# Performance work log

Measured on AMD Instinct MI355X. Metric: run time of the kernel, lower is better.

## Reference

```python
import jax, jax.numpy as jnp
import numpy as np

N_NODES = 16384
N_EDGES = 262144
N_GRAPHS = 64
COLORS = 16
EMB = 256
HEADS = 8
FFN = 1024
LAYERS = 4
LMAX = 320


def _ln(x, g, b, eps=1e-5):
    m = x.mean(-1, keepdims=True)
    v = x.var(-1, keepdims=True)
    return (x - m) * jax.lax.rsqrt(v + eps) * g + b


def setup_inputs() -> dict:
    key = jax.random.key(0)
    ks = iter(jax.random.split(key, 64))
    s = 0.05
    def rn(shape):
        return jax.random.normal(next(ks), shape, jnp.float32) * s
    # 64 graphs: 32 with 192 nodes, 32 with 320 nodes -> total 16384, L_max=320
    lengths = np.concatenate([np.full(32, 192, np.int64), np.full(32, 320, np.int64)])
    batches = jnp.asarray(np.concatenate([[0], np.cumsum(lengths)]).astype(np.int32))
    x = jax.random.normal(next(ks), (N_NODES, COLORS), jnp.float32)
    edge_index = jax.random.randint(next(ks), (2, N_EDGES), 0, N_NODES, jnp.int32)
    inp = dict(
        x=x, edge_index=edge_index, batches=batches, L_max=LMAX,
        sW0=rn((COLORS, EMB)), sWn0=rn((COLORS, EMB)), sb0=jnp.zeros(EMB),
        sW1=rn((EMB, EMB)), sWn1=rn((EMB, EMB)), sb1=jnp.zeros(EMB),
        sW2=rn((EMB, EMB)), sWn2=rn((EMB, EMB)), sb2=jnp.zeros(EMB),
        Wq=rn((LAYERS, EMB, EMB)), Wk=rn((LAYERS, EMB, EMB)), Wv=rn((LAYERS, EMB, EMB)),
        bq=jnp.zeros((LAYERS, EMB)), bk=jnp.zeros((LAYERS, EMB)), bv=jnp.zeros((LAYERS, EMB)),
        Wo=rn((LAYERS, EMB, EMB)), bo=jnp.zeros((LAYERS, EMB)),
        ln1g=jnp.ones((LAYERS, EMB)), ln1b=jnp.zeros((LAYERS, EMB)),
        ln2g=jnp.ones((LAYERS, EMB)), ln2b=jnp.zeros((LAYERS, EMB)),
        W1=rn((LAYERS, EMB, FFN)), b1=jnp.zeros((LAYERS, FFN)),
        W2=rn((LAYERS, FFN, EMB)), b2=jnp.zeros((LAYERS, EMB)),
    )
    return inp


def reference(x, edge_index, batches, L_max,
              sW0, sWn0, sb0, sW1, sWn1, sb1, sW2, sWn2, sb2,
              Wq, Wk, Wv, bq, bk, bv, Wo, bo,
              ln1g, ln1b, ln2g, ln2b, W1, b1, W2, b2):
    N = x.shape[0]
    src, dst = edge_index[0], edge_index[1]
    deg = jnp.maximum(
        jax.ops.segment_sum(jnp.ones(src.shape[0], x.dtype), dst, num_segments=N), 1.0
    )[:, None]

    def sage(h, Ws, Wn, b, act):
        agg = jax.ops.segment_sum(h[src], dst, num_segments=N) / deg  # mean neighbor agg
        h2 = h @ Ws + agg @ Wn + b
        return jax.nn.relu(h2) if act else h2

    z = sage(x, sW0, sWn0, sb0, True)
    z = sage(z, sW1, sWn1, sb1, True)
    z = sage(z, sW2, sWn2, sb2, False)

    # pack_and_pad (intended semantics): seq-first [L_max, n_graphs, D] + key padding mask
    nG = batches.shape[0] - 1
    lengths = batches[1:] - batches[:-1]
    ids = jnp.arange(N)
    seg = jnp.searchsorted(batches, ids, side='right') - 1  # graph id per node
    pos = ids - batches[seg]                                 # position within graph
    D = z.shape[1]
    h = jnp.zeros((L_max, nG, D), z.dtype).at[pos, seg].set(z)
    pad = jnp.arange(L_max)[None, :] >= lengths[:, None]     # [nG, L_max], True = padded

    H = HEADS
    dh = D // H
    scale = 1.0 / np.sqrt(dh).astype(np.float32)
    for l in range(Wq.shape[0]):
        L, Bg = h.shape[0], h.shape[1]
        q = (h @ Wq[l] + bq[l]).reshape(L, Bg, H, dh)
        k = (h @ Wk[l] + bk[l]).reshape(L, Bg, H, dh)
        v = (h @ Wv[l] + bv[l]).reshape(L, Bg, H, dh)
        sc = jnp.einsum('lbhd,mbhd->bhlm', q, k) * scale
        sc = jnp.where(pad[:, None, None, :], -1e9, sc)
        a = jax.nn.softmax(sc, axis=-1)
        o = jnp.einsum('bhlm,mbhd->lbhd', a, v).reshape(L, Bg, D) @ Wo[l] + bo[l]
        h = _ln(h + o, ln1g[l], ln1b[l])
        ff = jax.nn.relu(h @ W1[l] + b1[l]) @ W2[l] + b2[l]
        h = _ln(h + ff, ln2g[l], ln2b[l])
    return h
```

## Files before the change

### kernel.cpp

```cpp
#include <hip/hip_runtime.h>
#include <hip/hip_bf16.h>
#include <math.h>

#define NN  16384
#define NE  262144
#define NG  64
#define CIN 16
#define DD  256
#define NHD 8
#define DHD 32
#define DFF 1024
#define NLY 4
#define LM  320
#define QS  768
#define QKW 512
#define NV  16384
#define NRV 16512

typedef __attribute__((ext_vector_type(8))) short bf16x8;
typedef __attribute__((ext_vector_type(4))) float f32x4;

__device__ __forceinline__ unsigned short f2bf(float f) {
    union { __hip_bfloat16 h; unsigned short u; } cv;
    cv.h = __float2bfloat16(f);
    return cv.u;
}
__device__ __forceinline__ float bf2f(unsigned short u) {
    return __uint_as_float((unsigned int)u << 16);
}
__device__ __forceinline__ void gl_lds16(const unsigned short* g, unsigned short* l) {
    __builtin_amdgcn_global_load_lds(
        (const __attribute__((address_space(1))) unsigned int*)g,
        (__attribute__((address_space(3))) unsigned int*)l, 16, 0, 0);
}
__device__ __forceinline__ int gsearch(const int* __restrict__ batches, int row) {
    int lo = 0, hi = NG;
    while (lo < hi) {
        int mid = (lo + hi + 1) >> 1;
        if (batches[mid] <= row) lo = mid; else hi = mid - 1;
    }
    return lo;
}

__global__ __launch_bounds__(256) void prep_all_kernel(
    const float* __restrict__ Wq, const float* __restrict__ Wk, const float* __restrict__ Wv,
    const float* __restrict__ Wo, const float* __restrict__ W1, const float* __restrict__ W2,
    const float* __restrict__ sW1, const float* __restrict__ sWn1,
    const float* __restrict__ sW2, const float* __restrict__ sWn2,
    const float* __restrict__ bq, const float* __restrict__ bk, const float* __restrict__ bv,
    unsigned short* __restrict__ Wqkvt, unsigned short* __restrict__ Wot,
    unsigned short* __restrict__ W1t, unsigned short* __restrict__ W2t,
    unsigned short* __restrict__ sW1t, unsigned short* __restrict__ sWn1t,
    unsigned short* __restrict__ sW2t, unsigned short* __restrict__ sWn2t,
    float* __restrict__ bqkvp,
    uint4* __restrict__ hbz, uint4* __restrict__ obz, int* __restrict__ counts)
{
    const int t = threadIdx.x;
    int bid = blockIdx.x;
    if (bid < 12) {
        int i = bid * 256 + t;
        if (i < NLY * QS) {
            int n = i % QS, l = i / QS;
            const float* b = (n < 256) ? bq : (n < 512 ? bk : bv);
            float v = b[l * DD + (n & 255)];
            if (n < 256) v *= 0.17677669529663687f;
            bqkvp[i] = v;
        }
        return;
    }
    bid -= 12;
    if (bid >= 832) {
        int i = (bid - 832) * 256 + t;
        if (i < 4096) {
            hbz[i] = (uint4){0u, 0u, 0u, 0u};
            obz[i] = (uint4){0u, 0u, 0u, 0u};
        }
        if (i < NN) counts[i] = 0;
        return;
    }
    __shared__ float Ls[64][68];
    const float* inP;
    unsigned short* outP;
    int strideIn, strideOut;
    float sc = 1.f;
    if (bid < 192) {
        int x = bid % 12, y = (bid / 12) % 4, l = bid / 48;
        int n0 = x * 64, k0 = y * 64;
        const float* W = (n0 < 256) ? Wq : (n0 < 512 ? Wk : Wv);
        if (n0 < 256) sc = 0.17677669529663687f;
        inP  = W + ((size_t)l * DD + k0) * DD + (n0 & 255);
        strideIn = DD;
        outP = Wqkvt + ((size_t)l * QS + n0) * DD + k0;
        strideOut = DD;
    } else if (bid < 192 + 64) {
        bid -= 192;
        int x = bid % 4, y = (bid / 4) % 4, l = bid / 16;
        int n0 = x * 64, k0 = y * 64;
        inP  = Wo + ((size_t)l * DD + k0) * DD + n0;
        strideIn = DD;
        outP = Wot + ((size_t)l * DD + n0) * DD + k0;
        strideOut = DD;
    } else if (bid < 192 + 64 + 256) {
        bid -= 192 + 64;
        int x = bid % 16, y = (bid / 16) % 4, l = bid / 64;
        int n0 = x * 64, k0 = y * 64;
        inP  = W1 + ((size_t)l * DD + k0) * DFF + n0;
        strideIn = DFF;
        outP = W1t + ((size_t)l * DFF + n0) * DD + k0;
        strideOut = DD;
    } else if (bid < 192 + 64 + 512) {
        bid -= 192 + 64 + 256;
        int x = bid % 4, y = (bid / 4) % 16, l = bid / 64;
        int n0 = x * 64, k0 = y * 64;
        inP  = W2 + ((size_t)l * DFF + k0) * DD + n0;
        strideIn = DD;
        outP = W2t + ((size_t)l * DD + n0) * DFF + k0;
        strideOut = DFF;
    } else {
        bid -= 192 + 64 + 512;
        int w = bid / 16, r = bid % 16;
        int x = r % 4, y = r / 4;
        int n0 = x * 64, k0 = y * 64;
        const float* src = (w == 0) ? sW1 : (w == 1) ? sWn1 : (w == 2) ? sW2 : sWn2;
        unsigned short* dst = (w == 0) ? sW1t : (w == 1) ? sWn1t : (w == 2) ? sW2t : sWn2t;
        inP  = src + (size_t)k0 * DD + n0;
        strideIn = DD;
        outP = dst + (size_t)n0 * DD + k0;
        strideOut = DD;
    }
    #pragma unroll
    for (int it = 0; it < 4; ++it) {
        int lin = it * 256 + t;
        int kr = lin >> 4, nc = (lin & 15) * 4;
        float4 v = *(const float4*)&inP[(size_t)kr * strideIn + nc];
        Ls[kr][nc]     = v.x * sc;
        Ls[kr][nc + 1] = v.y * sc;
        Ls[kr][nc + 2] = v.z * sc;
        Ls[kr][nc + 3] = v.w * sc;
    }
    __syncthreads();
    #pragma unroll
    for (int it = 0; it < 2; ++it) {
        int lin = it * 256 + t;
        int nr = lin >> 3, kc = (lin & 7) * 8;
        unsigned short pk[8];
        #pragma unroll
        for (int j = 0; j < 8; ++j) pk[j] = f2bf(Ls[kc + j][nr]);
        *(uint4*)&outP[(size_t)nr * strideOut + kc] = *(uint4*)pk;
    }
}

__global__ void count_edges_kernel(const int* __restrict__ dst, int* __restrict__ counts) {
    int e = blockIdx.x * 256 + threadIdx.x;
    if (e < NE) atomicAdd(&counts[dst[e]], 1);
}

__global__ __launch_bounds__(1024) void scan_kernel(const int* __restrict__ counts,
                                                    int* __restrict__ offsets,
                                                    int* __restrict__ cursor) {
    __shared__ int part[1024];
    int t = threadIdx.x;
    int base = t * 16;
    int s = 0;
    #pragma unroll
    for (int i = 0; i < 16; ++i) s += counts[base + i];
    part[t] = s;
    __syncthreads();
    for (int off = 1; off < 1024; off <<= 1) {
        int val = (t >= off) ? part[t - off] : 0;
        __syncthreads();
        part[t] += val;
        __syncthreads();
    }
    int run = (t == 0) ? 0 : part[t - 1];
    #pragma unroll
    for (int i = 0; i < 16; ++i) {
        offsets[base + i] = run;
        cursor[base + i]  = run;
        run += counts[base + i];
    }
    if (t == 1023) offsets[NN] = run;
}

__global__ void fill_csr_kernel(const int* __restrict__ src, const int* __restrict__ dst,
                                int* __restrict__ cursor, int* __restrict__ csr) {
    int e = blockIdx.x * 256 + threadIdx.x;
    if (e < NE) {
        int p = atomicAdd(&cursor[dst[e]], 1);
        csr[p] = src[e];
    }
}

__global__ __launch_bounds__(256) void agg_mean16_kernel(
    const float* __restrict__ h, const int* __restrict__ offsets,
    const int* __restrict__ csr, float* __restrict__ out)
{
    int node = blockIdx.x * 16 + (threadIdx.x >> 4);
    int d = threadIdx.x & 15;
    int beg = offsets[node], end = offsets[node + 1];
    float acc = 0.f;
    int e = beg;
    for (; e + 3 < end; e += 4) {
        float v0 = h[(size_t)csr[e] * CIN + d];
        float v1 = h[(size_t)csr[e + 1] * CIN + d];
        float v2 = h[(size_t)csr[e + 2] * CIN + d];
        float v3 = h[(size_t)csr[e + 3] * CIN + d];
        acc += (v0 + v1) + (v2 + v3);
    }
    for (; e < end; ++e) acc += h[(size_t)csr[e] * CIN + d];
    int dg = end - beg; if (dg < 1) dg = 1;
    out[(size_t)node * CIN + d] = acc * (1.f / (float)dg);
}

__global__ __launch_bounds__(256) void agg_mean_b_kernel(
    const unsigned short* __restrict__ h, const int* __restrict__ offsets,
    const int* __restrict__ csr, unsigned short* __restrict__ out)
{
    int node = blockIdx.x * 4 + (threadIdx.x >> 6);
    int lane = threadIdx.x & 63;
    int half = lane >> 5;
    int hl   = lane & 31;
    int beg = offsets[node], end = offsets[node + 1];
    float a[8] = {0.f, 0.f, 0.f, 0.f, 0.f, 0.f, 0.f, 0.f};
    int e = beg + half;
    for (; e + 6 < end; e += 8) {
        bf16x8 h0 = *(const bf16x8*)(h + (size_t)csr[e]     * DD + hl * 8);
        bf16x8 h1 = *(const bf16x8*)(h + (size_t)csr[e + 2] * DD + hl * 8);
        bf16x8 h2 = *(const bf16x8*)(h + (size_t)csr[e + 4] * DD + hl * 8);
        bf16x8 h3 = *(const bf16x8*)(h + (size_t)csr[e + 6] * DD + hl * 8);
        #pragma unroll
        for (int j = 0; j < 8; ++j)
            a[j] += (bf2f((unsigned short)h0[j]) + bf2f((unsigned short)h1[j]))
                  + (bf2f((unsigned short)h2[j]) + bf2f((unsigned short)h3[j]));
    }
    for (; e < end; e += 2) {
        bf16x8 h0 = *(const bf16x8*)(h + (size_t)csr[e] * DD + hl * 8);
        #pragma unroll
        for (int j = 0; j < 8; ++j) a[j] += bf2f((unsigned short)h0[j]);
    }
    #pragma unroll
    for (int j = 0; j < 8; ++j) a[j] += __shfl_xor(a[j], 32, 64);
    int dg = end - beg; if (dg < 1) dg = 1;
    float inv = 1.f / (float)dg;
    if (half == 0) {
        unsigned short pk[8];
        #pragma unroll
        for (int j = 0; j < 8; ++j) pk[j] = f2bf(a[j] * inv);
        *(uint4*)(out + (size_t)node * DD + hl * 8) = *(uint4*)pk;
    }
}

template <int ACT, bool DUAL>
__global__ __launch_bounds__(256) void gemm_f32b_kernel(
    const float* __restrict__ A, const float* __restrict__ W,
    const float* __restrict__ A2, const float* __restrict__ W2,
    const float* __restrict__ bias, unsigned short* __restrict__ Cb,
    int M, int N, int K)
{
    __shared__ __align__(16) float As[16][64];
    __shared__ __align__(16) float Ws[16][64];
    const int t  = threadIdx.x;
    const int tx = t & 15, ty = t >> 4;
    const int m0 = blockIdx.y * 64, n0 = blockIdx.x * 64;
    const int arow = t >> 2, acol = (t & 3) * 4;
    const int wrow = t >> 4, wcol = (t & 15) * 4;
    float acc[4][4] = {};
    const int npass = DUAL ? 2 : 1;
    for (int pass = 0; pass < npass; ++pass) {
        const float* Ap = (DUAL && pass) ? A2 : A;
        const float* Wp = (DUAL && pass) ? W2 : W;
        for (int k0 = 0; k0 < K; k0 += 16) {
            __syncthreads();
            float4 av = *(const float4*)(Ap + (size_t)(m0 + arow) * K + k0 + acol);
            As[acol + 0][arow] = av.x;
            As[acol + 1][arow] = av.y;
            As[acol + 2][arow] = av.z;
            As[acol + 3][arow] = av.w;
            *(float4*)&Ws[wrow][wcol] = *(const float4*)(Wp + (size_t)(k0 + wrow) * N + n0 + wcol);
            __syncthreads();
            #pragma unroll
            for (int kk = 0; kk < 16; ++kk) {
                float4 a4 = *(const float4*)&As[kk][ty * 4];
                float4 b4 = *(const float4*)&Ws[kk][tx * 4];
                float aa[4] = {a4.x, a4.y, a4.z, a4.w};
                float bb[4] = {b4.x, b4.y, b4.z, b4.w};
                #pragma unroll
                for (int i = 0; i < 4; ++i)
                    #pragma unroll
                    for (int j = 0; j < 4; ++j)
                        acc[i][j] += aa[i] * bb[j];
            }
        }
    }
    float4 bv = *(const float4*)(bias + n0 + tx * 4);
    float bb4[4] = {bv.x, bv.y, bv.z, bv.w};
    #pragma unroll
    for (int i = 0; i < 4; ++i) {
        float c[4];
        #pragma unroll
        for (int j = 0; j < 4; ++j) {
            c[j] = acc[i][j] + bb4[j];
            if (ACT == 1) c[j] = fmaxf(c[j], 0.f);
        }
        ushort4 ov;
        ov.x = f2bf(c[0]); ov.y = f2bf(c[1]); ov.z = f2bf(c[2]); ov.w = f2bf(c[3]);
        *(ushort4*)(Cb + (size_t)(m0 + ty * 4 + i) * N + n0 + tx * 4) = ov;
    }
}

template <int ACT, bool DUAL>
__global__ __launch_bounds__(256) void mfma_gemm_kernel(
    const unsigned short* __restrict__ A,  const unsigned short* __restrict__ Wt,
    const unsigned short* __restrict__ A2, const unsigned short* __restrict__ Wt2,
    const float* __restrict__ bias, unsigned short* __restrict__ Cb,
    int M, int N, int K)
{
    __shared__ __align__(16) unsigned short As[128 * 64];
    __shared__ __align__(16) unsigned short Bs[128 * 64];
    const int t = threadIdx.x;
    const int wave = t >> 6, lane = t & 63;
    const int quad = lane >> 4, r16 = lane & 15;
    const int wr = (wave >> 1) * 64, wc = (wave & 1) * 64;
    const int m0 = blockIdx.y * 128, n0 = blockIdx.x * 128;
    const int srow = t >> 3;
    const int scol = ((t & 7) * 8) ^ ((srow & 7) << 3);
    const int swz  = (r16 & 7) << 3;

    f32x4 acc[4][4];
    #pragma unroll
    for (int i = 0; i < 4; ++i)
        #pragma unroll
        for (int j = 0; j < 4; ++j)
            acc[i][j] = (f32x4){0.f, 0.f, 0.f, 0.f};

    const int npass = DUAL ? 2 : 1;
    for (int pass = 0; pass < npass; ++pass) {
        const unsigned short* Ap = (DUAL && pass) ? A2 : A;
        const unsigned short* Wp = (DUAL && pass) ? Wt2 : Wt;
        for (int k0 = 0; k0 < K; k0 += 64) {
            __syncthreads();
            #pragma unroll
            for (int c = 0; c < 4; ++c) {
                gl_lds16(&Ap[(size_t)(m0 + c * 32 + srow) * K + k0 + scol],
                         As + c * 2048 + wave * 512);
                gl_lds16(&Wp[(size_t)(n0 + c * 32 + srow) * K + k0 + scol],
                         Bs + c * 2048 + wave * 512);
            }
            __syncthreads();
            #pragma unroll
            for (int kk = 0; kk < 2; ++kk) {
                const int cofs = (kk * 32 + quad * 8) ^ swz;
                bf16x8 af[4], bfr[4];
                #pragma unroll
                for (int i = 0; i < 4; ++i)
                    af[i] = *(const bf16x8*)&As[(wr + i * 16 + r16) * 64 + cofs];
                #pragma unroll
                for (int j = 0; j < 4; ++j)
                    bfr[j] = *(const bf16x8*)&Bs[(wc + j * 16 + r16) * 64 + cofs];
                #pragma unroll
                for (int i = 0; i < 4; ++i)
                    #pragma unroll
                    for (int j = 0; j < 4; ++j)
                        acc[i][j] = __builtin_amdgcn_mfma_f32_16x16x32_bf16(
                            af[i], bfr[j], acc[i][j], 0, 0, 0);
            }
        }
    }

    float bcol[4];
    #pragma unroll
    for (int j = 0; j < 4; ++j) bcol[j] = bias[n0 + wc + j * 16 + r16];
    #pragma unroll
    for (int i = 0; i < 4; ++i) {
        const int rowb = m0 + wr + i * 16 + quad * 4;
        #pragma unroll
        for (int rr = 0; rr < 4; ++rr) {
            const size_t rb = (size_t)(rowb + rr) * N;
            #pragma unroll
            for (int j = 0; j < 4; ++j) {
                float v = acc[i][j][rr] + bcol[j];
                if (ACT == 1) v = fmaxf(v, 0.f);
                Cb[rb + n0 + wc + j * 16 + r16] = f2bf(v);
            }
        }
    }
}

__global__ __launch_bounds__(256) void gemm_qkv_kernel(
    const unsigned short* __restrict__ A, const unsigned short* __restrict__ Wt,
    const float* __restrict__ bias, const int* __restrict__ batches,
    unsigned short* __restrict__ QKb, unsigned short* __restrict__ Vt, int K)
{
    __shared__ __align__(16) unsigned short As[128 * 64];
    __shared__ __align__(16) unsigned short Bs[128 * 64];
    const int t = threadIdx.x;
    const int wave = t >> 6, lane = t & 63;
    const int quad = lane >> 4, r16 = lane & 15;
    const int wr = (wave >> 1) * 64, wc = (wave & 1) * 64;
    const int m0 = blockIdx.y * 128, n0 = blockIdx.x * 128;
    const int srow = t >> 3;
    const int scol = ((t & 7) * 8) ^ ((srow & 7) << 3);
    const int swz  = (r16 & 7) << 3;

    f32x4 acc[4][4];
    #pragma unroll
    for (int i = 0; i < 4; ++i)
        #pragma unroll
        for (int j = 0; j < 4; ++j)
            acc[i][j] = (f32x4){0.f, 0.f, 0.f, 0.f};

    for (int k0 = 0; k0 < K; k0 += 64) {
        __syncthreads();
        #pragma unroll
        for (int c = 0; c < 4; ++c) {
            gl_lds16(&A[(size_t)(m0 + c * 32 + srow) * K + k0 + scol],
                     As + c * 2048 + wave * 512);
            gl_lds16(&Wt[(size_t)(n0 + c * 32 + srow) * K + k0 + scol],
                     Bs + c * 2048 + wave * 512);
        }
        __syncthreads();
        #pragma unroll
        for (int kk = 0; kk < 2; ++kk) {
            const int cofs = (kk * 32 + quad * 8) ^ swz;
            bf16x8 af[4], bfr[4];
            #pragma unroll
            for (int i = 0; i < 4; ++i)
                af[i] = *(const bf16x8*)&As[(wr + i * 16 + r16) * 64 + cofs];
            #pragma unroll
            for (int j = 0; j < 4; ++j)
                bfr[j] = *(const bf16x8*)&Bs[(wc + j * 16 + r16) * 64 + cofs];
            #pragma unroll
            for (int i = 0; i < 4; ++i)
                #pragma unroll
                for (int j = 0; j < 4; ++j)
                    acc[i][j] = __builtin_amdgcn_mfma_f32_16x16x32_bf16(
                        af[i], bfr[j], acc[i][j], 0, 0, 0);
        }
    }

    float bcol[4];
    #pragma unroll
    for (int j = 0; j < 4; ++j) bcol[j] = bias[n0 + wc + j * 16 + r16];

    if (n0 < 512) {
        #pragma unroll
        for (int i = 0; i < 4; ++i) {
            const int rowb = m0 + wr + i * 16 + quad * 4;
            #pragma unroll
            for (int rr = 0; rr < 4; ++rr) {
                const size_t rb = (size_t)(rowb + rr) * QKW;
                #pragma unroll
                for (int j = 0; j < 4; ++j)
                    QKb[rb + n0 + wc + j * 16 + r16] = f2bf(acc[i][j][rr] + bcol[j]);
            }
        }
    } else {
        #pragma unroll
        for (int i = 0; i < 4; ++i) {
            const int rowb = m0 + wr + i * 16 + quad * 4;
            if (rowb >= NV) continue;
            const int g = gsearch(batches, rowb);
            const int key = rowb - batches[g];
            #pragma unroll
            for (int j = 0; j < 4; ++j) {
                const int dim = n0 - 512 + wc + j * 16 + r16;
                unsigned short pk[4];
                #pragma unroll
                for (int rr = 0; rr < 4; ++rr) pk[rr] = f2bf(acc[i][j][rr] + bcol[j]);
                *(uint2*)&Vt[((size_t)g * DD + dim) * LM + key] = *(uint2*)pk;
            }
        }
    }
}

template <bool PERM>
__global__ __launch_bounds__(512) void gemm_ln_kernel(
    const unsigned short* __restrict__ A, const unsigned short* __restrict__ Wt,
    const float* __restrict__ bias, const unsigned short* __restrict__ residb,
    const float* __restrict__ gam, const float* __restrict__ bet,
    const int* __restrict__ batches,
    float* __restrict__ outF, float* __restrict__ repO,
    unsigned short* __restrict__ outHb, int K)
{
    __shared__ __align__(16) unsigned short As[64 * 64];
    __shared__ __align__(16) unsigned short Bs[256 * 64];
    __shared__ float red[2][4][64];
    const int t = threadIdx.x;
    const int wave = t >> 6, lane = t & 63;
    const int quad = lane >> 4, r16 = lane & 15;
    const int wr = (wave >> 2) * 32;
    const int wc = (wave & 3) * 64;
    const int m0 = blockIdx.x * 64;
    const int srow = t >> 3;
    const int scol = ((t & 7) * 8) ^ ((srow & 7) << 3);
    const int swz  = (r16 & 7) << 3;

    f32x4 acc[2][4];
    #pragma unroll
    for (int i = 0; i < 2; ++i)
        #pragma unroll
        for (int j = 0; j < 4; ++j)
            acc[i][j] = (f32x4){0.f, 0.f, 0.f, 0.f};

    for (int k0 = 0; k0 < K; k0 += 64) {
        __syncthreads();
        gl_lds16(&A[(size_t)(m0 + srow) * K + k0 + scol], As + wave * 512);
        #pragma unroll
        for (int c = 0; c < 4; ++c)
            gl_lds16(&Wt[(size_t)(c * 64 + srow) * K + k0 + scol],
                     Bs + c * 4096 + wave * 512);
        __syncthreads();
        #pragma unroll
        for (int kk = 0; kk < 2; ++kk) {
            const int cofs = (kk * 32 + quad * 8) ^ swz;
            bf16x8 af[2], bfr[4];
            #pragma unroll
            for (int i = 0; i < 2; ++i)
                af[i] = *(const bf16x8*)&As[(wr + i * 16 + r16) * 64 + cofs];
            #pragma unroll
            for (int j = 0; j < 4; ++j)
                bfr[j] = *(const bf16x8*)&Bs[(wc + j * 16 + r16) * 64 + cofs];
            #pragma unroll
            for (int i = 0; i < 2; ++i)
                #pragma unroll
                for (int j = 0; j < 4; ++j)
                    acc[i][j] = __builtin_amdgcn_mfma_f32_16x16x32_bf16(
                        af[i], bfr[j], acc[i][j], 0, 0, 0);
        }
    }

    float bcol[4];
    #pragma unroll
    for (int j = 0; j < 4; ++j) bcol[j] = bias[wc + j * 16 + r16];

    #pragma unroll
    for (int i = 0; i < 2; ++i) {
        const int row = wr + i * 16 + quad * 4;
        #pragma unroll
        for (int rr = 0; rr < 4; ++rr) {
            const size_t rb = (size_t)(m0 + row + rr) * DD;
            float s1 = 0.f, s2 = 0.f;
            #pragma unroll
            for (int j = 0; j < 4; ++j) {
                float v = acc[i][j][rr] + bcol[j] + bf2f(residb[rb + wc + j * 16 + r16]);
                acc[i][j][rr] = v;
                s1 += v;
                s2 += v * v;
            }
            #pragma unroll
            for (int off = 1; off < 16; off <<= 1) {
                s1 += __shfl_xor(s1, off, 64);
                s2 += __shfl_xor(s2, off, 64);
            }
            if (r16 == 0) {
                red[0][wave & 3][row + rr] = s1;
                red[1][wave & 3][row + rr] = s2;
            }
        }
    }
    __syncthreads();

    int gg = 0, posb = 0;
    if (PERM && m0 < NV) {
        gg = gsearch(batches, m0);
        posb = m0 - batches[gg];
    }
    #pragma unroll
    for (int i = 0; i < 2; ++i) {
        const int row = wr + i * 16 + quad * 4;
        #pragma unroll
        for (int rr = 0; rr < 4; ++rr) {
            const int lr = row + rr;
            const int gr = m0 + lr;
            float s1 = red[0][0][lr] + red[0][1][lr] + red[0][2][lr] + red[0][3][lr];
            float s2 = red[1][0][lr] + red[1][1][lr] + red[1][2][lr] + red[1][3][lr];
            float mean = s1 * (1.f / 256.f);
            float var  = s2 * (1.f / 256.f) - mean * mean;
            float rs = rsqrtf(var + 1e-5f);
            const size_t hb = (size_t)gr * DD;
            #pragma unroll
            for (int j = 0; j < 4; ++j) {
                const int col = wc + j * 16 + r16;
                float ov = (acc[i][j][rr] - mean) * rs * gam[col] + bet[col];
                if (PERM) {
                    if (m0 < NV) {
                        outF[((size_t)(posb + lr) * NG + gg) * DD + col] = ov;
                    } else {
                        int g2 = m0 - NV + lr;
                        if (g2 < NG) repO[(size_t)g2 * DD + col] = ov;
                    }
                } else {
                    outHb[hb + col] = f2bf(ov);
                }
            }
        }
    }
}

#define NBT ((NV / 64) * 2)
__global__ __launch_bounds__(256) void attn_kernel(
    const unsigned short* __restrict__ qk, const unsigned short* __restrict__ vt,
    const int* __restrict__ batches, unsigned short* __restrict__ o)
{
    __shared__ __align__(16) unsigned short Pa[4][64 * 40];
    const int bx = blockIdx.x;
    const int tid = threadIdx.x;
    const int wave = tid >> 6;
    const int lane = tid & 63;

    if (bx >= NBT) {
        float* pbuf = (float*)&Pa[wave][0];
        const int idx = (bx - NBT) * 4 + wave;
        const int g = idx >> 3, h = idx & 7;
        const int len = batches[g + 1] - batches[g];
        const size_t gq = (size_t)batches[g];

        float q[32];
        const unsigned short* qrow = qk + (size_t)(NV + g) * QKW + h * 32;
        #pragma unroll
        for (int c = 0; c < 4; ++c) {
            bf16x8 qv = *(const bf16x8*)(qrow + c * 8);
            #pragma unroll
            for (int j = 0; j < 8; ++j) q[c * 8 + j] = bf2f((unsigned short)qv[j]);
        }
        float psum = 0.f;
        for (int key = lane; key < len; key += 64) {
            const unsigned short* krow = qk + (gq + key) * QKW + 256 + h * 32;
            float s = 0.f;
            #pragma unroll
            for (int c = 0; c < 4; ++c) {
                bf16x8 kv = *(const bf16x8*)(krow + c * 8);
                #pragma unroll
                for (int j = 0; j < 8; ++j) s += q[c * 8 + j] * bf2f((unsigned short)kv[j]);
            }
            float pv = __expf(s);
            pbuf[key] = pv;
            psum += pv;
        }
        #pragma unroll
        for (int off = 1; off < 64; off <<= 1) psum += __shfl_xor(psum, off, 64);
        __asm__ volatile("s_waitcnt lgkmcnt(0)" ::: "memory");

        const int d = lane & 31, half = lane >> 5;
        float acc = 0.f;
        const unsigned short* vrow = vt + ((size_t)g * DD + h * 32 + d) * LM;
        for (int key = half * 8; key < len; key += 16) {
            bf16x8 v8 = *(const bf16x8*)(vrow + key);
            #pragma unroll
            for (int j = 0; j < 8; ++j) acc += pbuf[key + j] * bf2f((unsigned short)v8[j]);
        }
        acc += __shfl_xor(acc, 32, 64);
        if (half == 0)
            o[(size_t)(NV + g) * DD + h * 32 + d] = f2bf(acc / psum);
        return;
    }

    const int tile = bx >> 1;
    const int row0 = tile * 64;
    const int h = (bx & 1) * 4 + wave;
    const int quad = lane >> 4, r16 = lane & 15;
    const int g = gsearch(batches, row0);
    const int len = batches[g + 1] - batches[g];
    const size_t gq = (size_t)batches[g];
    unsigned short* pa = Pa[wave];

    bf16x8 qf[4];
    #pragma unroll
    for (int i = 0; i < 4; ++i)
        qf[i] = *(const bf16x8*)(qk + (size_t)(row0 + i * 16 + r16) * QKW + h * 32 + quad * 8);
    bf16x8 onesf;
    #pragma unroll
    for (int j = 0; j < 8; ++j) onesf[j] = (short)0x3F80;

    f32x4 oacc[4][2], lacc[4];
    #pragma unroll
    for (int i = 0; i < 4; ++i) {
        lacc[i] = (f32x4){0.f, 0.f, 0.f, 0.f};
        #pragma unroll
        for (int nt = 0; nt < 2; ++nt)
            oacc[i][nt] = (f32x4){0.f, 0.f, 0.f, 0.f};
    }

    const unsigned short* kbase = qk + gq * QKW + 256 + h * 32 + quad * 8;
    const unsigned short* vbase = vt + ((size_t)g * DD + h * 32 + r16) * LM + quad * 8;

    bf16x8 kf[2], vf[2];
    kf[0] = *(const bf16x8*)(kbase + (size_t)(r16) * QKW);
    kf[1] = *(const bf16x8*)(kbase + (size_t)(16 + r16) * QKW);
    vf[0] = *(const bf16x8*)(vbase);
    vf[1] = *(const bf16x8*)(vbase + 16 * LM);

    for (int t0 = 0; t0 < len; t0 += 32) {
        f32x4 st[2][4];
        #pragma unroll
        for (int mt = 0; mt < 2; ++mt)
            #pragma unroll
            for (int i = 0; i < 4; ++i)
                st[mt][i] = (f32x4){0.f, 0.f, 0.f, 0.f};
        __builtin_amdgcn_s_setprio(1);
        #pragma unroll
        for (int mt = 0; mt < 2; ++mt)
            #pragma unroll
            for (int i = 0; i < 4; ++i)
                st[mt][i] = __builtin_amdgcn_mfma_f32_16x16x32_bf16(
                    kf[mt], qf[i], st[mt][i], 0, 0, 0);
        __builtin_amdgcn_s_setprio(0);

        const bool more = (t0 + 32) < len;
        bf16x8 kn[2], vn[2];
        if (more) {
            const int tn = t0 + 32;
            kn[0] = *(const bf16x8*)(kbase + (size_t)(tn + r16) * QKW);
            kn[1] = *(const bf16x8*)(kbase + (size_t)(tn + 16 + r16) * QKW);
            vn[0] = *(const bf16x8*)(vbase + tn);
            vn[1] = *(const bf16x8*)(vbase + 16 * LM + tn);
        }

        #pragma unroll
        for (int i = 0; i < 4; ++i) {
            #pragma unroll
            for (int mt = 0; mt < 2; ++mt) {
                float pr[4];
                #pragma unroll
                for (int rr = 0; rr < 4; ++rr)
                    pr[rr] = __expf(st[mt][i][rr]);
                uint2 w;
                w.x = ((unsigned)f2bf(pr[1]) << 16) | f2bf(pr[0]);
                w.y = ((unsigned)f2bf(pr[3]) << 16) | f2bf(pr[2]);
                *(uint2*)&pa[(i * 16 + r16) * 40 + mt * 16 + quad * 4] = w;
            }
        }
        __asm__ volatile("s_waitcnt lgkmcnt(0)" ::: "memory");
        bf16x8 pf[4];
        #pragma unroll
        for (int i = 0; i < 4; ++i)
            pf[i] = *(const bf16x8*)&pa[(i * 16 + r16) * 40 + quad * 8];
        __builtin_amdgcn_s_setprio(1);
        #pragma unroll
        for (int i = 0; i < 4; ++i) {
            #pragma unroll
            for (int nt = 0; nt < 2; ++nt)
                oacc[i][nt] = __builtin_amdgcn_mfma_f32_16x16x32_bf16(
                    pf[i], vf[nt], oacc[i][nt], 0, 0, 0);
            lacc[i] = __builtin_amdgcn_mfma_f32_16x16x32_bf16(
                pf[i], onesf, lacc[i], 0, 0, 0);
        }
        __builtin_amdgcn_s_setprio(0);
        if (more) {
            kf[0] = kn[0]; kf[1] = kn[1];
            vf[0] = vn[0]; vf[1] = vn[1];
        }
    }
    #pragma unroll
    for (int i = 0; i < 4; ++i) {
        #pragma unroll
        for (int rr = 0; rr < 4; ++rr) {
            float inv = 1.f / lacc[i][rr];
            size_t base = (size_t)(row0 + i * 16 + quad * 4 + rr) * DD + h * 32;
            #pragma unroll
            for (int nt = 0; nt < 2; ++nt)
                o[base + nt * 16 + r16] = f2bf(oacc[i][nt][rr] * inv);
        }
    }
}

__global__ __launch_bounds__(256) void bcast_pad_kernel(
    const float* __restrict__ repO, const int* __restrict__ batches,
    float* __restrict__ outF)
{
    const int g = blockIdx.x;
    const int t = threadIdx.x;
    const int len = batches[g + 1] - batches[g];
    float v = repO[(size_t)g * DD + t];
    for (int pos = len; pos < LM; ++pos)
        outF[((size_t)pos * NG + g) * DD + t] = v;
}

extern "C" void kernel_launch(void* const* d_in, const int* in_sizes, int n_in,
                              void* d_out, int out_size, void* d_ws, size_t ws_size,
                              hipStream_t stream) {
    const float* x       = (const float*)d_in[0];
    const int*   ei      = (const int*)d_in[1];
    const int*   batches = (const int*)d_in[2];
    const float* sW0  = (const float*)d_in[4];
    const float* sWn0 = (const float*)d_in[5];
    const float* sb0  = (const float*)d_in[6];
    const float* sW1  = (const float*)d_in[7];
    const float* sWn1 = (const float*)d_in[8];
    const float* sb1  = (const float*)d_in[9];
    const float* sW2  = (const float*)d_in[10];
    const float* sWn2 = (const float*)d_in[11];
    const float* sb2  = (const float*)d_in[12];
    const float* Wq   = (const float*)d_in[13];
    const float* Wk   = (const float*)d_in[14];
    const float* Wv   = (const float*)d_in[15];
    const float* bq   = (const float*)d_in[16];
    const float* bk   = (const float*)d_in[17];
    const float* bv   = (const float*)d_in[18];
    const float* Wo   = (const float*)d_in[19];
    const float* bo   = (const float*)d_in[20];
    const float* ln1g = (const float*)d_in[21];
    const float* ln1b = (const float*)d_in[22];
    const float* ln2g = (const float*)d_in[23];
    const float* ln2b = (const float*)d_in[24];
    const float* W1   = (const float*)d_in[25];
    const float* b1   = (const float*)d_in[26];
    const float* W2   = (const float*)d_in[27];
    const float* b2   = (const float*)d_in[28];

    char* p = (char*)d_ws;
    auto alloc = [&](size_t bytes) {
        char* r = p;
        p += (bytes + 255) & ~(size_t)255;
        return r;
    };
    int*   counts  = (int*)alloc((size_t)NN * 4);
    int*   offsets = (int*)alloc((size_t)(NN + 1) * 4);
    int*   cursor  = (int*)alloc((size_t)NN * 4);
    int*   csr     = (int*)alloc((size_t)NE * 4);
    float* agg0    = (float*)alloc((size_t)NN * CIN * 4);
    unsigned short* z0b = (unsigned short*)alloc((size_t)NN * DD * 2);
    unsigned short* a1b = (unsigned short*)alloc((size_t)NN * DD * 2);
    unsigned short* z1b = (unsigned short*)alloc((size_t)NN * DD * 2);
    unsigned short* a2b = (unsigned short*)alloc((size_t)NN * DD * 2);
    unsigned short* Vt = (unsigned short*)alloc((size_t)NG * DD * LM * 2);
    unsigned short* Hb = (unsigned short*)alloc((size_t)NRV * DD * 2);
    unsigned short* Ob = (unsigned short*)alloc((size_t)NRV * DD * 2);
    unsigned short* R  = (unsigned short*)alloc((size_t)NRV * DFF * 2);
    unsigned short* QKb = R;
    unsigned short* F1b = R;
    unsigned short* Wqkvt = (unsigned short*)alloc((size_t)NLY * QS * DD * 2);
    unsigned short* Wot   = (unsigned short*)alloc((size_t)NLY * DD * DD * 2);
    unsigned short* W1t   = (unsigned short*)alloc((size_t)NLY * DFF * DD * 2);
    unsigned short* W2t   = (unsigned short*)alloc((size_t)NLY * DD * DFF * 2);
    unsigned short* sW1t  = (unsigned short*)alloc((size_t)DD * DD * 2);
    unsigned short* sWn1t = (unsigned short*)alloc((size_t)DD * DD * 2);
    unsigned short* sW2t  = (unsigned short*)alloc((size_t)DD * DD * 2);
    unsigned short* sWn2t = (unsigned short*)alloc((size_t)DD * DD * 2);
    float* bqkvp   = (float*)alloc((size_t)NLY * QS * 4);
    float* repOut  = (float*)alloc((size_t)NG * DD * 4);

    prep_all_kernel<<<908, 256, 0, stream>>>(
        Wq, Wk, Wv, Wo, W1, W2, sW1, sWn1, sW2, sWn2, bq, bk, bv,
        Wqkvt, Wot, W1t, W2t, sW1t, sWn1t, sW2t, sWn2t, bqkvp,
        (uint4*)(Hb + (size_t)NV * DD), (uint4*)(Ob + (size_t)NV * DD), counts);

    count_edges_kernel<<<NE / 256, 256, 0, stream>>>(ei + NE, counts);
    scan_kernel<<<1, 1024, 0, stream>>>(counts, offsets, cursor);
    fill_csr_kernel<<<NE / 256, 256, 0, stream>>>(ei, ei + NE, cursor, csr);

    agg_mean16_kernel<<<NN / 16, 256, 0, stream>>>(x, offsets, csr, agg0);
    gemm_f32b_kernel<1, true><<<dim3(DD / 64, NN / 64), 256, 0, stream>>>(
        x, sW0, agg0, sWn0, sb0, z0b, NN, DD, CIN);
    agg_mean_b_kernel<<<NN / 4, 256, 0, stream>>>(z0b, offsets, csr, a1b);
    mfma_gemm_kernel<1, true><<<dim3(DD / 128, NN / 128), 256, 0, stream>>>(
        z0b, sW1t, a1b, sWn1t, sb1, z1b, NN, DD, DD);
    agg_mean_b_kernel<<<NN / 4, 256, 0, stream>>>(z1b, offsets, csr, a2b);
    mfma_gemm_kernel<0, true><<<dim3(DD / 128, NN / 128), 256, 0, stream>>>(
        z1b, sW2t, a2b, sWn2t, sb2, Hb, NN, DD, DD);

    for (int l = 0; l < NLY; ++l) {
        gemm_qkv_kernel<<<dim3(QS / 128, NRV / 128), 256, 0, stream>>>(
            Hb, Wqkvt + (size_t)l * QS * DD, bqkvp + (size_t)l * QS, batches, QKb, Vt, DD);
        attn_kernel<<<NBT + NG * 2, 256, 0, stream>>>(QKb, Vt, batches, Ob);
        gemm_ln_kernel<false><<<NRV / 64, 512, 0, stream>>>(
            Ob, Wot + (size_t)l * DD * DD, bo + (size_t)l * DD, Hb,
            ln1g + (size_t)l * DD, ln1b + (size_t)l * DD, batches, nullptr, nullptr, Hb, DD);
        mfma_gemm_kernel<1, false><<<dim3(DFF / 128, NRV / 128), 256, 0, stream>>>(
            Hb, W1t + (size_t)l * DFF * DD, nullptr, nullptr,
            b1 + (size_t)l * DFF, F1b, NRV, DFF, DD);
        if (l == NLY - 1)
            gemm_ln_kernel<true><<<NRV / 64, 512, 0, stream>>>(
                F1b, W2t + (size_t)l * DD * DFF, b2 + (size_t)l * DD, Hb,
                ln2g + (size_t)l * DD, ln2b + (size_t)l * DD, batches,
                (float*)d_out, repOut, Hb, DFF);
        else
            gemm_ln_kernel<false><<<NRV / 64, 512, 0, stream>>>(
                F1b, W2t + (size_t)l * DD * DFF, b2 + (size_t)l * DD, Hb,
                ln2g + (size_t)l * DD, ln2b + (size_t)l * DD, batches,
                nullptr, nullptr, Hb, DFF);
    }
    bcast_pad_kernel<<<NG, 256, 0, stream>>>(repOut, batches, (float*)d_out);
}
```

Before: 669.5 us.

## Double-buffer LDS tiles in MFMA GEMM kernels to overlap loads with compute

Converts the three MFMA GEMM kernels (generic, QKV, and GEMM+LayerNorm) from single-buffered LDS tiles to ping-pong double buffering. The next K-tile is loaded into LDS with direct global-to-LDS loads while MFMAs run on the current tile. One vmcnt wait plus a barrier per iteration replaces the two __syncthreads. This hides global load latency but doubles LDS use per block (64KB for the 128x128 kernels, larger for the LN kernel), which may reduce occupancy.

```diff
diff --git a/kernel.cpp b/kernel.cpp
--- a/kernel.cpp
+++ b/kernel.cpp
@@ -315,8 +315,8 @@
     const float* __restrict__ bias, unsigned short* __restrict__ Cb,
     int M, int N, int K)
 {
-    __shared__ __align__(16) unsigned short As[128 * 64];
-    __shared__ __align__(16) unsigned short Bs[128 * 64];
+    __shared__ __align__(16) unsigned short As[2][128 * 64];
+    __shared__ __align__(16) unsigned short Bs[2][128 * 64];
     const int t = threadIdx.x;
     const int wave = t >> 6, lane = t & 63;
     const int quad = lane >> 4, r16 = lane & 15;
@@ -325,6 +325,8 @@
     const int srow = t >> 3;
     const int scol = ((t & 7) * 8) ^ ((srow & 7) << 3);
     const int swz  = (r16 & 7) << 3;
+    const int ks = K >> 6;
+    const int nt = DUAL ? ks * 2 : ks;
 
     f32x4 acc[4][4];
     #pragma unroll
@@ -333,38 +335,47 @@
         for (int j = 0; j < 4; ++j)
             acc[i][j] = (f32x4){0.f, 0.f, 0.f, 0.f};
 
-    const int npass = DUAL ? 2 : 1;
-    for (int pass = 0; pass < npass; ++pass) {
-        const unsigned short* Ap = (DUAL && pass) ? A2 : A;
-        const unsigned short* Wp = (DUAL && pass) ? Wt2 : Wt;
-        for (int k0 = 0; k0 < K; k0 += 64) {
-            __syncthreads();
-            #pragma unroll
-            for (int c = 0; c < 4; ++c) {
-                gl_lds16(&Ap[(size_t)(m0 + c * 32 + srow) * K + k0 + scol],
-                         As + c * 2048 + wave * 512);
-                gl_lds16(&Wp[(size_t)(n0 + c * 32 + srow) * K + k0 + scol],
-                         Bs + c * 2048 + wave * 512);
-            }
-            __syncthreads();
-            #pragma unroll
-            for (int kk = 0; kk < 2; ++kk) {
-                const int cofs = (kk * 32 + quad * 8) ^ swz;
-                bf16x8 af[4], bfr[4];
-                #pragma unroll
-                for (int i = 0; i < 4; ++i)
-                    af[i] = *(const bf16x8*)&As[(wr + i * 16 + r16) * 64 + cofs];
+    auto stage = [&](int buf, int kt) {
+        const unsigned short* Ap = A;
+        const unsigned short* Wp = Wt;
+        int kq = kt;
+        if (DUAL && kt >= ks) { Ap = A2; Wp = Wt2; kq = kt - ks; }
+        const int k0 = kq << 6;
+        #pragma unroll
+        for (int c = 0; c < 4; ++c) {
+            gl_lds16(&Ap[(size_t)(m0 + c * 32 + srow) * K + k0 + scol],
+                     &As[buf][c * 2048 + wave * 512]);
+            gl_lds16(&Wp[(size_t)(n0 + c * 32 + srow) * K + k0 + scol],
+                     &Bs[buf][c * 2048 + wave * 512]);
+        }
+    };
+
+    stage(0, 0);
+    __asm__ volatile("s_waitcnt vmcnt(0)" ::: "memory");
+    __builtin_amdgcn_s_barrier();
+    int cur = 0;
+    for (int kt = 0; kt < nt; ++kt) {
+        if (kt + 1 < nt) stage(cur ^ 1, kt + 1);
+        #pragma unroll
+        for (int kk = 0; kk < 2; ++kk) {
+            const int cofs = (kk * 32 + quad * 8) ^ swz;
+            bf16x8 af[4], bfr[4];
+            #pragma unroll
+            for (int i = 0; i < 4; ++i)
+                af[i] = *(const bf16x8*)&As[cur][(wr + i * 16 + r16) * 64 + cofs];
+            #pragma unroll
+            for (int j = 0; j < 4; ++j)
+                bfr[j] = *(const bf16x8*)&Bs[cur][(wc + j * 16 + r16) * 64 + cofs];
+            #pragma unroll
+            for (int i = 0; i < 4; ++i)
                 #pragma unroll
                 for (int j = 0; j < 4; ++j)
-                    bfr[j] = *(const bf16x8*)&Bs[(wc + j * 16 + r16) * 64 + cofs];
-                #pragma unroll
-                for (int i = 0; i < 4; ++i)
-                    #pragma unroll
-                    for (int j = 0; j < 4; ++j)
-                        acc[i][j] = __builtin_amdgcn_mfma_f32_16x16x32_bf16(
-                            af[i], bfr[j], acc[i][j], 0, 0, 0);
-            }
-        }
+                    acc[i][j] = __builtin_amdgcn_mfma_f32_16x16x32_bf16(
+                        af[i], bfr[j], acc[i][j], 0, 0, 0);
+        }
+        __asm__ volatile("s_waitcnt vmcnt(0)" ::: "memory");
+        __builtin_amdgcn_s_barrier();
+        cur ^= 1;
     }
 
     float bcol[4];
@@ -391,8 +402,8 @@
     const float* __restrict__ bias, const int* __restrict__ batches,
     unsigned short* __restrict__ QKb, unsigned short* __restrict__ Vt, int K)
 {
-    __shared__ __align__(16) unsigned short As[128 * 64];
-    __shared__ __align__(16) unsigned short Bs[128 * 64];
+    __shared__ __align__(16) unsigned short As[2][128 * 64];
+    __shared__ __align__(16) unsigned short Bs[2][128 * 64];
     const int t = threadIdx.x;
     const int wave = t >> 6, lane = t & 63;
     const int quad = lane >> 4, r16 = lane & 15;
@@ -401,6 +412,7 @@
     const int srow = t >> 3;
     const int scol = ((t & 7) * 8) ^ ((srow & 7) << 3);
     const int swz  = (r16 & 7) << 3;
+    const int nt = K >> 6;
 
     f32x4 acc[4][4];
     #pragma unroll
@@ -409,26 +421,33 @@
         for (int j = 0; j < 4; ++j)
             acc[i][j] = (f32x4){0.f, 0.f, 0.f, 0.f};
 
-    for (int k0 = 0; k0 < K; k0 += 64) {
-        __syncthreads();
+    auto stage = [&](int buf, int kt) {
+        const int k0 = kt << 6;
         #pragma unroll
         for (int c = 0; c < 4; ++c) {
             gl_lds16(&A[(size_t)(m0 + c * 32 + srow) * K + k0 + scol],
-                     As + c * 2048 + wave * 512);
+                     &As[buf][c * 2048 + wave * 512]);
             gl_lds16(&Wt[(size_t)(n0 + c * 32 + srow) * K + k0 + scol],
-                     Bs + c * 2048 + wave * 512);
-        }
-        __syncthreads();
+                     &Bs[buf][c * 2048 + wave * 512]);
+        }
+    };
+
+    stage(0, 0);
+    __asm__ volatile("s_waitcnt vmcnt(0)" ::: "memory");
+    __builtin_amdgcn_s_barrier();
+    int cur = 0;
+    for (int kt = 0; kt < nt; ++kt) {
+        if (kt + 1 < nt) stage(cur ^ 1, kt + 1);
         #pragma unroll
         for (int kk = 0; kk < 2; ++kk) {
             const int cofs = (kk * 32 + quad * 8) ^ swz;
             bf16x8 af[4], bfr[4];
             #pragma unroll
             for (int i = 0; i < 4; ++i)
-                af[i] = *(const bf16x8*)&As[(wr + i * 16 + r16) * 64 + cofs];
+                af[i] = *(const bf16x8*)&As[cur][(wr + i * 16 + r16) * 64 + cofs];
             #pragma unroll
             for (int j = 0; j < 4; ++j)
-                bfr[j] = *(const bf16x8*)&Bs[(wc + j * 16 + r16) * 64 + cofs];
+                bfr[j] = *(const bf16x8*)&Bs[cur][(wc + j * 16 + r16) * 64 + cofs];
             #pragma unroll
             for (int i = 0; i < 4; ++i)
                 #pragma unroll
@@ -436,6 +455,9 @@
                     acc[i][j] = __builtin_amdgcn_mfma_f32_16x16x32_bf16(
                         af[i], bfr[j], acc[i][j], 0, 0, 0);
         }
+        __asm__ volatile("s_waitcnt vmcnt(0)" ::: "memory");
+        __builtin_amdgcn_s_barrier();
+        cur ^= 1;
     }
 
     float bcol[4];
@@ -482,8 +504,8 @@
     float* __restrict__ outF, float* __restrict__ repO,
     unsigned short* __restrict__ outHb, int K)
 {
-    __shared__ __align__(16) unsigned short As[64 * 64];
-    __shared__ __align__(16) unsigned short Bs[256 * 64];
+    __shared__ __align__(16) unsigned short As[2][64 * 64];
+    __shared__ __align__(16) unsigned short Bs[2][256 * 64];
     __shared__ float red[2][4][64];
     const int t = threadIdx.x;
     const int wave = t >> 6, lane = t & 63;
@@ -494,6 +516,7 @@
     const int srow = t >> 3;
     const int scol = ((t & 7) * 8) ^ ((srow & 7) << 3);
     const int swz  = (r16 & 7) << 3;
+    const int nt = K >> 6;
 
     f32x4 acc[2][4];
     #pragma unroll
@@ -502,24 +525,31 @@
         for (int j = 0; j < 4; ++j)
             acc[i][j] = (f32x4){0.f, 0.f, 0.f, 0.f};
 
-    for (int k0 = 0; k0 < K; k0 += 64) {
-        __syncthreads();
-        gl_lds16(&A[(size_t)(m0 + srow) * K + k0 + scol], As + wave * 512);
+    auto stage = [&](int buf, int kt) {
+        const int k0 = kt << 6;
+        gl_lds16(&A[(size_t)(m0 + srow) * K + k0 + scol], &As[buf][wave * 512]);
         #pragma unroll
         for (int c = 0; c < 4; ++c)
             gl_lds16(&Wt[(size_t)(c * 64 + srow) * K + k0 + scol],
-                     Bs + c * 4096 + wave * 512);
-        __syncthreads();
+                     &Bs[buf][c * 4096 + wave * 512]);
+    };
+
+    stage(0, 0);
+    __asm__ volatile("s_waitcnt vmcnt(0)" ::: "memory");
+    __builtin_amdgcn_s_barrier();
+    int cur = 0;
+    for (int kt = 0; kt < nt; ++kt) {
+        if (kt + 1 < nt) stage(cur ^ 1, kt + 1);
         #pragma unroll
         for (int kk = 0; kk < 2; ++kk) {
             const int cofs = (kk * 32 + quad * 8) ^ swz;
             bf16x8 af[2], bfr[4];
             #pragma unroll
             for (int i = 0; i < 2; ++i)
-                af[i] = *(const bf16x8*)&As[(wr + i * 16 + r16) * 64 + cofs];
+                af[i] = *(const bf16x8*)&As[cur][(wr + i * 16 + r16) * 64 + cofs];
             #pragma unroll
             for (int j = 0; j < 4; ++j)
-                bfr[j] = *(const bf16x8*)&Bs[(wc + j * 16 + r16) * 64 + cofs];
+                bfr[j] = *(const bf16x8*)&Bs[cur][(wc + j * 16 + r16) * 64 + cofs];
             #pragma unroll
             for (int i = 0; i < 2; ++i)
                 #pragma unroll
@@ -527,6 +557,9 @@
                     acc[i][j] = __builtin_amdgcn_mfma_f32_16x16x32_bf16(
                         af[i], bfr[j], acc[i][j], 0, 0, 0);
         }
+        __asm__ volatile("s_waitcnt vmcnt(0)" ::: "memory");
+        __builtin_amdgcn_s_barrier();
+        cur ^= 1;
     }
 
     float bcol[4];
```

Measured after the change: 773.7 us. 1.16x slower.
